# Performance work log

Hardware: AMD Instinct MI355X
Metric: run time of the kernel (lower is better)

## Reference

```python
import jax, jax.numpy as jnp
import numpy as np
from jax import lax

EPS = 1e-12


def _conv_block(x, w, scale, bias, pool):
    # x: (N, Cin, H, W), w: (Cout, Cin, 3, 3). BN in eval mode folded into scale/bias.
    y = lax.conv_general_dilated(x, w, window_strides=(1, 1), padding='SAME',
                                 dimension_numbers=('NCHW', 'OIHW', 'NCHW'))
    y = y * scale[None, :, None, None] + bias[None, :, None, None]
    y = jax.nn.relu(y)
    if pool:
        y = lax.reduce_window(y, -jnp.inf, lax.max, (1, 1, 2, 2), (1, 1, 2, 2), 'VALID')
    return y


def _encoder(x, w1, s1, b1, w2, s2, b2, w3, s3, b3, w4, s4, b4):
    x = _conv_block(x, w1, s1, b1, True)
    x = _conv_block(x, w2, s2, b2, True)
    x = _conv_block(x, w3, s3, b3, False)
    x = _conv_block(x, w4, s4, b4, False)
    return x  # (N, 64, 21, 21)


def _l2norm(x, axis):
    n = jnp.sqrt(jnp.sum(x * x, axis=axis, keepdims=True))
    return x / jnp.maximum(n, EPS)


def setup_inputs() -> dict:
    key = jax.random.key(0)
    ks = jax.random.split(key, 8)
    B, NQ, Way, Shot, C, H, W = 2, 75, 5, 5, 3, 84, 84
    D = 64
    inp = {
        'query': jax.random.normal(ks[0], (B, NQ, C, H, W), jnp.float32),
        'support': jax.random.normal(ks[1], (B, Way, Shot, C, H, W), jnp.float32),
        'w1': jax.random.normal(ks[2], (D, C, 3, 3), jnp.float32) * 0.1,
        'w2': jax.random.normal(ks[3], (D, D, 3, 3), jnp.float32) * 0.05,
        'w3': jax.random.normal(ks[4], (D, D, 3, 3), jnp.float32) * 0.05,
        'w4': jax.random.normal(ks[5], (D, D, 3, 3), jnp.float32) * 0.05,
    }
    for i in range(1, 5):
        inp[f's{i}'] = jnp.ones((D,), jnp.float32)
        inp[f'b{i}'] = jnp.zeros((D,), jnp.float32)
    return inp


def reference(query, support, w1, s1, b1, w2, s2, b2, w3, s3, b3, w4, s4, b4):
    B, NQ, C, H, W = query.shape
    _, Way, Shot, _, _, _ = support.shape
    q_flat = query.reshape(B * NQ, C, H, W)
    s_flat = support.reshape(B * Way * Shot, C, H, W)
    q_feat = _encoder(q_flat, w1, s1, b1, w2, s2, b2, w3, s3, b3, w4, s4, b4)
    s_feat = _encoder(s_flat, w1, s1, b1, w2, s2, b2, w3, s3, b3, w4, s4, b4)
    D, h, w = q_feat.shape[1], q_feat.shape[2], q_feat.shape[3]
    HW = h * w
    q_local = _l2norm(q_feat.reshape(B, NQ, D, HW), axis=2)            # (B,NQ,D,HW)
    s_local = s_feat.reshape(B, Way, Shot, D, HW).mean(axis=2)          # mean over shots
    s_local = _l2norm(s_local, axis=2)                                  # (B,Way,D,HW)
    # all pairwise local cosine similarities, batched in one einsum
    sim = jnp.einsum('bqdm,bcdn->bqcmn', q_local, s_local)              # (B,NQ,Way,HW,HW)
    best = sim.max(axis=-1)                                             # best match per query descriptor
    scores = best.mean(axis=-1)                                         # (B,NQ,Way)
    return scores.reshape(B * NQ, Way)
```

## Files before the change

### kernel.cpp

```cpp
#include <hip/hip_runtime.h>

#define EPS 1e-12f

#define NIMG   200
#define NQIMG  150
#define BDIM   2
#define NQ     75
#define WAY    5
#define SHOT   5
#define DCH    64
#define H1     84
#define H2     42
#define H3     21
#define HW1    7056
#define HW2    1764
#define HW3    441
#define PH     86
#define PSZ    7396
#define SST    448

#define PAD_BLKS  4334
#define W1_BLKS   8
#define W_BLKS    432

typedef __attribute__((ext_vector_type(8))) short bf16x8;
typedef __attribute__((ext_vector_type(4))) float f32x4;

__device__ __forceinline__ unsigned short f2bf(float f) {
    unsigned u = __float_as_uint(f);
    u += 0x7fffu + ((u >> 16) & 1u);
    return (unsigned short)(u >> 16);
}
__device__ __forceinline__ float bf2f(unsigned short h) {
    return __uint_as_float(((unsigned)h) << 16);
}
__device__ __forceinline__ int swz(int pix, int c) {
    return pix * 128 + ((c ^ ((pix >> 1) & 7)) << 4);
}

__global__ __launch_bounds__(256) void prep(
    const float* __restrict__ qin, const float* __restrict__ sin_,
    const float* __restrict__ w1, const float* __restrict__ s1,
    const float* __restrict__ w2, const float* __restrict__ s2,
    const float* __restrict__ w3, const float* __restrict__ s3,
    const float* __restrict__ w4, const float* __restrict__ s4,
    unsigned short* __restrict__ pad, unsigned short* __restrict__ p1,
    unsigned short* __restrict__ p2, unsigned short* __restrict__ p3,
    unsigned short* __restrict__ p4)
{
    int blk = blockIdx.x;
    if (blk < PAD_BLKS) {
        int idx4 = blk * 256 + threadIdx.x;
        if (idx4 >= NIMG * 3 * PSZ / 4) return;
        int idx = idx4 * 4;
        int img = idx / (3 * PSZ);
        int rem = idx % (3 * PSZ);
        int ci = rem / PSZ, p = rem % PSZ;
        const float* src = (img < NQIMG) ? (qin + (size_t)img * 3 * HW1)
                                         : (sin_ + (size_t)(img - NQIMG) * 3 * HW1);
        unsigned short o[4];
        #pragma unroll
        for (int e = 0; e < 4; e++) {
            int pe = p + e;
            int iy = pe / PH, ix = pe % PH;
            float v = 0.f;
            if (iy >= 1 && iy <= H1 && ix >= 1 && ix <= H1)
                v = src[(size_t)ci * HW1 + (iy - 1) * H1 + (ix - 1)];
            o[e] = f2bf(v);
        }
        uint2 pk;
        pk.x = (unsigned)o[0] | ((unsigned)o[1] << 16);
        pk.y = (unsigned)o[2] | ((unsigned)o[3] << 16);
        *reinterpret_cast<uint2*>(pad + idx) = pk;
    } else if (blk < PAD_BLKS + W1_BLKS) {
        int idx = (blk - PAD_BLKS) * 256 + threadIdx.x;
        int j = idx & 7, lane = (idx >> 3) & 63, mt = idx >> 9;
        int co = (mt << 4) + (lane & 15);
        int k = ((lane >> 4) << 3) + j;
        float v = 0.f;
        if (k < 27) {
            int ci = k / 9, s = k % 9;
            v = w1[(co * 3 + ci) * 9 + s] * s1[co];
        }
        p1[idx] = f2bf(v);
    } else {
        int idx = (blk - PAD_BLKS - W1_BLKS) * 256 + threadIdx.x;
        int which = idx / 36864;
        int r = idx % 36864;
        int j = r & 7, lane = (r >> 3) & 63, mt = (r >> 9) & 3, t = (r >> 11) & 1, s = r >> 12;
        int co = (mt << 4) + (lane & 15);
        int ci = (t << 5) + ((lane >> 4) << 3) + j;
        const float* w = (which == 0) ? w2 : (which == 1) ? w3 : w4;
        const float* sc = (which == 0) ? s2 : (which == 1) ? s3 : s4;
        unsigned short* p = (which == 0) ? p2 : (which == 1) ? p3 : p4;
        p[r] = f2bf(w[(co * 64 + ci) * 9 + s] * sc[co]);
    }
}

__global__ __launch_bounds__(256) void conv12_fused(
    const unsigned short* __restrict__ pad,
    const unsigned short* __restrict__ wp1, const float* __restrict__ bias1,
    const unsigned short* __restrict__ wp2, const float* __restrict__ bias2,
    unsigned short* __restrict__ out)
{
    int img = blockIdx.x / 7, tg = blockIdx.x % 7;
    int tid = threadIdx.x;
    __shared__ __attribute__((aligned(16))) unsigned short strip[3 * 18 * 86];
    __shared__ unsigned short lds2[352 * DCH];

    const unsigned* srcd = (const unsigned*)pad;
    size_t ibase = (size_t)img * 3 * (PSZ / 2);
    #pragma unroll
    for (int it = 0; it < 10; it++) {
        int i = it * 256 + tid;
        if (i < 2322) {
            int ci = i / 774, rem = i % 774;
            int sr = rem / 43, d = rem % 43;
            int y = 12 * tg - 3 + sr;
            unsigned v = 0;
            if (y >= -1 && y <= 84)
                v = srcd[ibase + ci * 3698 + (y + 1) * 43 + d];
            ((unsigned*)strip)[ci * 774 + sr * 43 + d] = v;
        }
    }
    __syncthreads();

    int wv = tid >> 6, lane = tid & 63;
    int lc = lane & 15, kg = lane >> 4;

    {
        const bf16x8* w1v = (const bf16x8*)wp1;
        bf16x8 a0 = w1v[lane];
        bf16x8 a1 = w1v[64 + lane];
        bf16x8 a2 = w1v[128 + lane];
        bf16x8 a3 = w1v[192 + lane];

        int off[8];
        #pragma unroll
        for (int j = 0; j < 8; j++) {
            int k = (kg << 3) + j;
            int kk = k < 27 ? k : 0;
            int ci = kk / 9, s = kk % 9;
            off[j] = ci * 1548 + (s / 3) * 86 + (s % 3);
        }

        f32x4 bini[4];
        #pragma unroll
        for (int mt = 0; mt < 4; mt++) {
            float4 bq = *reinterpret_cast<const float4*>(bias1 + (mt << 4) + (kg << 2));
            bini[mt] = (f32x4){bq.x, bq.y, bq.z, bq.w};
        }

        #pragma unroll
        for (int rnd = 0; rnd < 6; rnd++) {
            int pl = rnd * 64 + wv * 16 + lc;
            bool instrip = pl < 352;
            int plc = instrip ? pl : 0;
            int rr = plc / 44, cc = plc % 44;
            int pr = 6 * tg - 1 + rr, pc = cc - 1;
            bool validpx = instrip && ((unsigned)pr < (unsigned)H2) && ((unsigned)pc < (unsigned)H2);
            int ccc = ((unsigned)pc < (unsigned)H2) ? cc : 1;
            int base = (2 * rr) * 86 + (2 * ccc - 2);

            bf16x8 b[4];
            #pragma unroll
            for (int j = 0; j < 8; j++) {
                int a = base + off[j];
                b[0][j] = (short)strip[a];
                b[1][j] = (short)strip[a + 1];
                b[2][j] = (short)strip[a + 86];
                b[3][j] = (short)strip[a + 87];
            }

            f32x4 acc[4][4];
            #pragma unroll
            for (int mt = 0; mt < 4; mt++)
                #pragma unroll
                for (int sub = 0; sub < 4; sub++)
                    acc[mt][sub] = bini[mt];
            #pragma unroll
            for (int sub = 0; sub < 4; sub++) {
                acc[0][sub] = __builtin_amdgcn_mfma_f32_16x16x32_bf16(a0, b[sub], acc[0][sub], 0, 0, 0);
                acc[1][sub] = __builtin_amdgcn_mfma_f32_16x16x32_bf16(a1, b[sub], acc[1][sub], 0, 0, 0);
                acc[2][sub] = __builtin_amdgcn_mfma_f32_16x16x32_bf16(a2, b[sub], acc[2][sub], 0, 0, 0);
                acc[3][sub] = __builtin_amdgcn_mfma_f32_16x16x32_bf16(a3, b[sub], acc[3][sub], 0, 0, 0);
            }

            if (instrip) {
                #pragma unroll
                for (int mt = 0; mt < 4; mt++) {
                    uint2 pk = make_uint2(0u, 0u);
                    if (validpx) {
                        unsigned short uo[4];
                        #pragma unroll
                        for (int r = 0; r < 4; r++) {
                            float m = fmaxf(fmaxf(acc[mt][0][r], acc[mt][1][r]),
                                            fmaxf(acc[mt][2][r], acc[mt][3][r]));
                            uo[r] = f2bf(fmaxf(m, 0.f));
                        }
                        pk.x = (unsigned)uo[0] | ((unsigned)uo[1] << 16);
                        pk.y = (unsigned)uo[2] | ((unsigned)uo[3] << 16);
                    }
                    int c = (mt << 1) + (kg >> 1);
                    *(uint2*)((char*)lds2 + swz(pl, c) + ((kg & 1) << 3)) = pk;
                }
            }
        }
    }
    __syncthreads();

    int p_local = wv * 16 + lc;
    bool valid = p_local < 63;
    int pl = valid ? p_local : 62;
    int pyl = pl / 21, pxl = pl % 21;
    int pixc[4];
    #pragma unroll
    for (int sub = 0; sub < 4; sub++)
        pixc[sub] = (2 * pyl + (sub >> 1) + 1) * 44 + (2 * pxl + (sub & 1) + 1);

    f32x4 bini[4];
    #pragma unroll
    for (int mt = 0; mt < 4; mt++) {
        float4 bq = *reinterpret_cast<const float4*>(bias2 + (mt << 4) + (kg << 2));
        bini[mt] = (f32x4){bq.x, bq.y, bq.z, bq.w};
    }

    const bf16x8* wvv = (const bf16x8*)wp2;
    f32x4 acc[4][4];
    #pragma unroll
    for (int i = 0; i < 4; i++)
        #pragma unroll
        for (int j = 0; j < 4; j++)
            acc[i][j] = bini[i];

    for (int s = 0; s < 9; s++) {
        int offs = (s / 3 - 1) * 44 + (s % 3 - 1);
        #pragma unroll
        for (int t = 0; t < 2; t++) {
            int fbase = ((s * 2 + t) * 4) << 6;
            bf16x8 a0 = wvv[fbase + lane];
            bf16x8 a1 = wvv[fbase + 64 + lane];
            bf16x8 a2 = wvv[fbase + 128 + lane];
            bf16x8 a3 = wvv[fbase + 192 + lane];
            int c = (t << 2) + kg;
            bf16x8 b[4];
            #pragma unroll
            for (int sub = 0; sub < 4; sub++) {
                int pix = pixc[sub] + offs;
                b[sub] = *(const bf16x8*)((const char*)lds2 + swz(pix, c));
            }
            #pragma unroll
            for (int sub = 0; sub < 4; sub++) {
                acc[0][sub] = __builtin_amdgcn_mfma_f32_16x16x32_bf16(a0, b[sub], acc[0][sub], 0, 0, 0);
                acc[1][sub] = __builtin_amdgcn_mfma_f32_16x16x32_bf16(a1, b[sub], acc[1][sub], 0, 0, 0);
                acc[2][sub] = __builtin_amdgcn_mfma_f32_16x16x32_bf16(a2, b[sub], acc[2][sub], 0, 0, 0);
                acc[3][sub] = __builtin_amdgcn_mfma_f32_16x16x32_bf16(a3, b[sub], acc[3][sub], 0, 0, 0);
            }
        }
    }

    if (!valid) return;
    int p = tg * 63 + p_local;
    #pragma unroll
    for (int mt = 0; mt < 4; mt++) {
        unsigned short uo[4];
        #pragma unroll
        for (int r = 0; r < 4; r++) {
            float m = fmaxf(fmaxf(acc[mt][0][r], acc[mt][1][r]),
                            fmaxf(acc[mt][2][r], acc[mt][3][r]));
            uo[r] = f2bf(fmaxf(m, 0.f));
        }
        uint2 pk;
        pk.x = (unsigned)uo[0] | ((unsigned)uo[1] << 16);
        pk.y = (unsigned)uo[2] | ((unsigned)uo[3] << 16);
        *reinterpret_cast<uint2*>(out + ((size_t)img * HW3 + p) * DCH + (mt << 4) + (kg << 2)) = pk;
    }
}

__global__ __launch_bounds__(256) void conv34_fused(
    const unsigned short* __restrict__ act,
    const unsigned short* __restrict__ wp3, const unsigned short* __restrict__ wp4,
    const float* __restrict__ b3, const float* __restrict__ b4,
    unsigned short* __restrict__ a4out,
    unsigned short* __restrict__ qlout)
{
    int img = blockIdx.x;
    int tid = threadIdx.x;
    __shared__ unsigned short lds[529 * DCH];

    const unsigned short* ab = act + (size_t)img * HW3 * DCH;
    #pragma unroll
    for (int it = 0; it < 17; it++) {
        int idx = it * 256 + tid;
        if (idx < 529 * 8) {
            int pix = idx >> 3, c = idx & 7;
            int r = pix / 23, xx = pix % 23;
            int y = r - 1, x = xx - 1;
            bf16x8 v = (bf16x8)(short)0;
            if ((unsigned)y < (unsigned)H3 && (unsigned)x < (unsigned)H3)
                v = *(const bf16x8*)(ab + ((size_t)(y * H3 + x)) * DCH + (c << 3));
            *(bf16x8*)((char*)lds + swz(pix, c)) = v;
        }
    }
    __syncthreads();

    int wv = tid >> 6, lane = tid & 63;
    int lc = lane & 15, kg = lane >> 4;
    int pixBase[7];
    bool pv[7];
    #pragma unroll
    for (int i = 0; i < 7; i++) {
        int p = (wv * 7 + i) * 16 + lc;
        pv[i] = p < HW3;
        int pc = pv[i] ? p : HW3 - 1;
        pixBase[i] = (pc / 21) * 23 + (pc % 21);
    }

    f32x4 bini[4];
    #pragma unroll
    for (int mt = 0; mt < 4; mt++) {
        float4 bq = *reinterpret_cast<const float4*>(b3 + (mt << 4) + (kg << 2));
        bini[mt] = (f32x4){bq.x, bq.y, bq.z, bq.w};
    }

    f32x4 acc[7][4];
    #pragma unroll
    for (int i = 0; i < 7; i++)
        #pragma unroll
        for (int m = 0; m < 4; m++)
            acc[i][m] = bini[m];

    const bf16x8* wv3 = (const bf16x8*)wp3;
    for (int s = 0; s < 9; s++) {
        int offs = (s / 3) * 23 + (s % 3);
        #pragma unroll
        for (int t = 0; t < 2; t++) {
            int fbase = ((s * 2 + t) * 4) << 6;
            bf16x8 a0 = wv3[fbase + lane];
            bf16x8 a1 = wv3[fbase + 64 + lane];
            bf16x8 a2 = wv3[fbase + 128 + lane];
            bf16x8 a3 = wv3[fbase + 192 + lane];
            int c = (t << 2) + kg;
            #pragma unroll
            for (int i = 0; i < 7; i++) {
                int pix = pixBase[i] + offs;
                bf16x8 bb = *(const bf16x8*)((const char*)lds + swz(pix, c));
                acc[i][0] = __builtin_amdgcn_mfma_f32_16x16x32_bf16(a0, bb, acc[i][0], 0, 0, 0);
                acc[i][1] = __builtin_amdgcn_mfma_f32_16x16x32_bf16(a1, bb, acc[i][1], 0, 0, 0);
                acc[i][2] = __builtin_amdgcn_mfma_f32_16x16x32_bf16(a2, bb, acc[i][2], 0, 0, 0);
                acc[i][3] = __builtin_amdgcn_mfma_f32_16x16x32_bf16(a3, bb, acc[i][3], 0, 0, 0);
            }
        }
    }

    __syncthreads();

    #pragma unroll
    for (int i = 0; i < 7; i++) {
        if (!pv[i]) continue;
        int pix = pixBase[i] + 24;
        #pragma unroll
        for (int mt = 0; mt < 4; mt++) {
            unsigned short uo[4];
            #pragma unroll
            for (int r = 0; r < 4; r++)
                uo[r] = f2bf(fmaxf(acc[i][mt][r], 0.f));
            uint2 pk;
            pk.x = (unsigned)uo[0] | ((unsigned)uo[1] << 16);
            pk.y = (unsigned)uo[2] | ((unsigned)uo[3] << 16);
            int c = (mt << 1) + (kg >> 1);
            *(uint2*)((char*)lds + swz(pix, c) + ((kg & 1) << 3)) = pk;
        }
    }
    #pragma unroll
    for (int it = 0; it < 3; it++) {
        int idx = it * 256 + tid;
        if (idx < 704) {
            int j = idx >> 3, c = idx & 7;
            int pix;
            if (j < 23)      pix = j;
            else if (j < 46) pix = 506 + (j - 23);
            else { int k = j - 46; pix = (1 + (k >> 1)) * 23 + (k & 1) * 22; }
            *(bf16x8*)((char*)lds + swz(pix, c)) = (bf16x8)(short)0;
        }
    }
    __syncthreads();

    #pragma unroll
    for (int mt = 0; mt < 4; mt++) {
        float4 bq = *reinterpret_cast<const float4*>(b4 + (mt << 4) + (kg << 2));
        bini[mt] = (f32x4){bq.x, bq.y, bq.z, bq.w};
    }
    #pragma unroll
    for (int i = 0; i < 7; i++)
        #pragma unroll
        for (int m = 0; m < 4; m++)
            acc[i][m] = bini[m];

    const bf16x8* wv4 = (const bf16x8*)wp4;
    for (int s = 0; s < 9; s++) {
        int offs = (s / 3) * 23 + (s % 3);
        #pragma unroll
        for (int t = 0; t < 2; t++) {
            int fbase = ((s * 2 + t) * 4) << 6;
            bf16x8 a0 = wv4[fbase + lane];
            bf16x8 a1 = wv4[fbase + 64 + lane];
            bf16x8 a2 = wv4[fbase + 128 + lane];
            bf16x8 a3 = wv4[fbase + 192 + lane];
            int c = (t << 2) + kg;
            #pragma unroll
            for (int i = 0; i < 7; i++) {
                int pix = pixBase[i] + offs;
                bf16x8 bb = *(const bf16x8*)((const char*)lds + swz(pix, c));
                acc[i][0] = __builtin_amdgcn_mfma_f32_16x16x32_bf16(a0, bb, acc[i][0], 0, 0, 0);
                acc[i][1] = __builtin_amdgcn_mfma_f32_16x16x32_bf16(a1, bb, acc[i][1], 0, 0, 0);
                acc[i][2] = __builtin_amdgcn_mfma_f32_16x16x32_bf16(a2, bb, acc[i][2], 0, 0, 0);
                acc[i][3] = __builtin_amdgcn_mfma_f32_16x16x32_bf16(a3, bb, acc[i][3], 0, 0, 0);
            }
        }
    }

    if (img < NQIMG) {
        #pragma unroll
        for (int i = 0; i < 7; i++) {
            float v[4][4];
            float ssq = 0.f;
            #pragma unroll
            for (int mt = 0; mt < 4; mt++)
                #pragma unroll
                for (int r = 0; r < 4; r++) {
                    float x = fmaxf(acc[i][mt][r], 0.f);
                    v[mt][r] = x;
                    ssq = fmaf(x, x, ssq);
                }
            ssq += __shfl_xor(ssq, 16, 64);
            ssq += __shfl_xor(ssq, 32, 64);
            float inv = 1.f / fmaxf(sqrtf(ssq), EPS);
            if (!pv[i]) continue;
            int p = (wv * 7 + i) * 16 + lc;
            #pragma unroll
            for (int mt = 0; mt < 4; mt++) {
                unsigned short uo[4];
                #pragma unroll
                for (int r = 0; r < 4; r++)
                    uo[r] = f2bf(v[mt][r] * inv);
                uint2 pk;
                pk.x = (unsigned)uo[0] | ((unsigned)uo[1] << 16);
                pk.y = (unsigned)uo[2] | ((unsigned)uo[3] << 16);
                *reinterpret_cast<uint2*>(qlout + ((size_t)img * HW3 + p) * DCH + (mt << 4) + (kg << 2)) = pk;
            }
        }
    } else {
        #pragma unroll
        for (int mt = 0; mt < 4; mt++) {
            #pragma unroll
            for (int i = 0; i < 7; i++) {
                if (!pv[i]) continue;
                int p = (wv * 7 + i) * 16 + lc;
                unsigned short uo[4];
                #pragma unroll
                for (int r = 0; r < 4; r++)
                    uo[r] = f2bf(fmaxf(acc[i][mt][r], 0.f));
                uint2 pk;
                pk.x = (unsigned)uo[0] | ((unsigned)uo[1] << 16);
                pk.y = (unsigned)uo[2] | ((unsigned)uo[3] << 16);
                *reinterpret_cast<uint2*>(a4out + ((size_t)img * HW3 + p) * DCH + (mt << 4) + (kg << 2)) = pk;
            }
        }
    }
}

__global__ __launch_bounds__(256) void s_mean_norm(
    const unsigned short* __restrict__ feat, unsigned short* __restrict__ s_local)
{
    int idx = blockIdx.x * 256 + threadIdx.x;
    if (idx >= BDIM * WAY * SST) return;
    int hw = idx % SST;
    int bc = idx / SST;
    bf16x8* o = (bf16x8*)(s_local + (size_t)idx * DCH);
    if (hw >= HW3) {
        #pragma unroll
        for (int g = 0; g < 8; g++) o[g] = (bf16x8)(short)0;
        return;
    }
    int img0 = NQIMG + bc * SHOT;
    float v[DCH];
    #pragma unroll
    for (int d = 0; d < DCH; d++) v[d] = 0.f;
    for (int sh = 0; sh < SHOT; sh++) {
        const bf16x8* f = (const bf16x8*)(feat + ((size_t)(img0 + sh) * HW3 + hw) * DCH);
        #pragma unroll
        for (int g = 0; g < 8; g++) {
            bf16x8 x = f[g];
            #pragma unroll
            for (int j = 0; j < 8; j++)
                v[g * 8 + j] += bf2f((unsigned short)x[j]);
        }
    }
    float ss = 0.f;
    #pragma unroll
    for (int d = 0; d < DCH; d++) {
        v[d] *= (1.f / SHOT);
        ss = fmaf(v[d], v[d], ss);
    }
    float inv = 1.f / fmaxf(sqrtf(ss), EPS);
    #pragma unroll
    for (int g = 0; g < 8; g++) {
        bf16x8 pk;
        #pragma unroll
        for (int j = 0; j < 8; j++) pk[j] = (short)f2bf(v[g * 8 + j] * inv);
        o[g] = pk;
    }
}

__global__ __launch_bounds__(256) void sim_mfma(
    const unsigned short* __restrict__ qloc,
    const unsigned short* __restrict__ sloc,
    float* __restrict__ out)
{
    int blk = blockIdx.x;
    int imgq = blk / WAY, way = blk % WAY;
    int b = imgq / NQ;
    const unsigned short* qp = qloc + (size_t)imgq * HW3 * DCH;
    const unsigned short* sp = sloc + (size_t)(b * WAY + way) * SST * DCH;

    __shared__ unsigned short slds[SST * DCH];
    int tid = threadIdx.x;
    #pragma unroll
    for (int it = 0; it < 14; it++) {
        int idx = it * 256 + tid;
        int pix = idx >> 3, c = idx & 7;
        bf16x8 v = *(const bf16x8*)(sp + ((size_t)pix << 6) + (c << 3));
        *(bf16x8*)((char*)slds + swz(pix, c)) = v;
    }
    __syncthreads();

    int wv = tid >> 6, lane = tid & 63;
    int lc = lane & 15, kg = lane >> 4;
    int mt0 = wv * 7;

    bf16x8 qa0[7], qa1[7];
    #pragma unroll
    for (int i = 0; i < 7; i++) {
        const unsigned short* qrow = qp + (size_t)((mt0 + i) * 16 + lc) * DCH + (kg << 3);
        qa0[i] = *(const bf16x8*)(qrow);
        qa1[i] = *(const bf16x8*)(qrow + 32);
    }
    f32x4 rmax[7];
    #pragma unroll
    for (int i = 0; i < 7; i++)
        rmax[i] = (f32x4){-1e30f, -1e30f, -1e30f, -1e30f};

    const f32x4 z4 = (f32x4){0.f, 0.f, 0.f, 0.f};

    #pragma unroll
    for (int g = 0; g < 6; g++) {
        bf16x8 s0[4], s1[4];
        #pragma unroll
        for (int u = 0; u < 4; u++) {
            int pix = (4 * g + u) * 16 + lc;
            s0[u] = *(const bf16x8*)((const char*)slds + swz(pix, kg));
            s1[u] = *(const bf16x8*)((const char*)slds + swz(pix, 4 + kg));
        }
        #pragma unroll
        for (int i = 0; i < 7; i++) {
            f32x4 a[4];
            #pragma unroll
            for (int u = 0; u < 4; u++) {
                a[u] = __builtin_amdgcn_mfma_f32_16x16x32_bf16(qa0[i], s0[u], z4, 0, 0, 0);
                a[u] = __builtin_amdgcn_mfma_f32_16x16x32_bf16(qa1[i], s1[u], a[u], 0, 0, 0);
            }
            #pragma unroll
            for (int r = 0; r < 4; r++) {
                float t = fmaxf(fmaxf(rmax[i][r], a[0][r]), a[1][r]);
                rmax[i][r] = fmaxf(fmaxf(t, a[2][r]), a[3][r]);
            }
        }
    }
    {
        bf16x8 s0[4], s1[4];
        #pragma unroll
        for (int u = 0; u < 4; u++) {
            int pix = (24 + u) * 16 + lc;
            s0[u] = *(const bf16x8*)((const char*)slds + swz(pix, kg));
            s1[u] = *(const bf16x8*)((const char*)slds + swz(pix, 4 + kg));
        }
        bool nval = (432 + lc) < HW3;
        #pragma unroll
        for (int i = 0; i < 7; i++) {
            f32x4 a[4];
            #pragma unroll
            for (int u = 0; u < 4; u++) {
                a[u] = __builtin_amdgcn_mfma_f32_16x16x32_bf16(qa0[i], s0[u], z4, 0, 0, 0);
                a[u] = __builtin_amdgcn_mfma_f32_16x16x32_bf16(qa1[i], s1[u], a[u], 0, 0, 0);
            }
            #pragma unroll
            for (int r = 0; r < 4; r++) {
                float t = fmaxf(fmaxf(rmax[i][r], a[0][r]), a[1][r]);
                rmax[i][r] = fmaxf(fmaxf(t, a[2][r]), nval ? a[3][r] : -1e30f);
            }
        }
    }

    float msum = 0.f;
    #pragma unroll
    for (int i = 0; i < 7; i++) {
        #pragma unroll
        for (int r = 0; r < 4; r++) {
            float v = rmax[i][r];
            v = fmaxf(v, __shfl_xor(v, 1, 64));
            v = fmaxf(v, __shfl_xor(v, 2, 64));
            v = fmaxf(v, __shfl_xor(v, 4, 64));
            v = fmaxf(v, __shfl_xor(v, 8, 64));
            int m = (mt0 + i) * 16 + (kg << 2) + r;
            if (lc == 0 && m < HW3) msum += v;
        }
    }
    #pragma unroll
    for (int off = 32; off > 0; off >>= 1)
        msum += __shfl_xor(msum, off, 64);
    __shared__ float red[4];
    if (lane == 0) red[wv] = msum;
    __syncthreads();
    if (tid == 0)
        out[(size_t)imgq * WAY + way] = (red[0] + red[1] + red[2] + red[3]) * (1.f / HW3);
}

extern "C" void kernel_launch(void* const* d_in, const int* in_sizes, int n_in,
                              void* d_out, int out_size, void* d_ws, size_t ws_size,
                              hipStream_t stream) {
    const float* query   = (const float*)d_in[0];
    const float* support = (const float*)d_in[1];
    const float* w1 = (const float*)d_in[2];
    const float* w2 = (const float*)d_in[3];
    const float* w3 = (const float*)d_in[4];
    const float* w4 = (const float*)d_in[5];
    const float* s1 = (const float*)d_in[6];
    const float* b1 = (const float*)d_in[7];
    const float* s2 = (const float*)d_in[8];
    const float* b2 = (const float*)d_in[9];
    const float* s3 = (const float*)d_in[10];
    const float* b3 = (const float*)d_in[11];
    const float* s4 = (const float*)d_in[12];
    const float* b4 = (const float*)d_in[13];
    float* out = (float*)d_out;

    char* ws = (char*)d_ws;
    unsigned short* A2  = (unsigned short*)(ws);
    unsigned short* A4  = (unsigned short*)(ws + 11289600);
    unsigned short* QL  = (unsigned short*)(ws + 22579200);
    unsigned short* SL  = (unsigned short*)(ws + 31046400);
    unsigned short* WP2 = (unsigned short*)(ws + 31619840);
    unsigned short* WP3 = (unsigned short*)(ws + 31693568);
    unsigned short* WP4 = (unsigned short*)(ws + 31767296);
    unsigned short* WP1 = (unsigned short*)(ws + 31841024);
    unsigned short* PAD = (unsigned short*)(ws + 31845120);

    prep<<<PAD_BLKS + W1_BLKS + W_BLKS, 256, 0, stream>>>(
        query, support, w1, s1, w2, s2, w3, s3, w4, s4, PAD, WP1, WP2, WP3, WP4);

    conv12_fused<<<NIMG * 7, 256, 0, stream>>>(PAD, WP1, b1, WP2, b2, A2);
    conv34_fused<<<NIMG, 256, 0, stream>>>(A2, WP3, WP4, b3, b4, A4, QL);

    s_mean_norm<<<(BDIM * WAY * SST + 255) / 256, 256, 0, stream>>>(A4, SL);

    sim_mfma<<<NQIMG * WAY, 256, 0, stream>>>(QL, SL, out);
}
```

Measured before the change: 127.8 us.

## Use dword LDS gathers for conv1 im2col and reuse a 4x4 input window in conv2

For conv1, a second copy of the input strip is built in LDS, shifted by one bf16 element. Every tap can then be fetched as an aligned 32-bit load that yields two adjacent pixels, replacing the per-element 16-bit LDS reads. For conv2, the loop order changes to channel-half outer and tap inner. A 4x4 window of input vectors is loaded once per channel half and reused across all 9 taps and 4 pool positions, cutting 72 LDS loads per thread down to 32. This costs more LDS (the shifted strip copy), an extra barrier, and more registers held live for the window.

```diff
diff --git a/kernel.cpp b/kernel.cpp
--- a/kernel.cpp
+++ b/kernel.cpp
@@ -18,6 +18,7 @@
 #define PH     86
 #define PSZ    7396
 #define SST    448
+#define SLEN   4648
 
 #define PAD_BLKS  4334
 #define W1_BLKS   8
@@ -25,6 +26,7 @@
 
 typedef __attribute__((ext_vector_type(8))) short bf16x8;
 typedef __attribute__((ext_vector_type(4))) float f32x4;
+typedef __attribute__((ext_vector_type(4))) unsigned u32x4;
 
 __device__ __forceinline__ unsigned short f2bf(float f) {
     unsigned u = __float_as_uint(f);
@@ -105,8 +107,11 @@
 {
     int img = blockIdx.x / 7, tg = blockIdx.x % 7;
     int tid = threadIdx.x;
-    __shared__ __attribute__((aligned(16))) unsigned short strip[3 * 18 * 86];
+    __shared__ __attribute__((aligned(16))) unsigned short strips[2 * SLEN];
     __shared__ unsigned short lds2[352 * DCH];
+
+    unsigned* s_dw  = (unsigned*)strips;
+    unsigned* sB_dw = (unsigned*)(strips + SLEN);
 
     const unsigned* srcd = (const unsigned*)pad;
     size_t ibase = (size_t)img * 3 * (PSZ / 2);
@@ -120,7 +125,17 @@
             unsigned v = 0;
             if (y >= -1 && y <= 84)
                 v = srcd[ibase + ci * 3698 + (y + 1) * 43 + d];
-            ((unsigned*)strip)[ci * 774 + sr * 43 + d] = v;
+            s_dw[i] = v;
+        }
+    }
+    __syncthreads();
+    #pragma unroll
+    for (int it = 0; it < 10; it++) {
+        int k = it * 256 + tid;
+        if (k < 2322) {
+            unsigned lo = s_dw[k];
+            unsigned hi = (k + 1 < 2322) ? s_dw[k + 1] : 0u;
+            sB_dw[k] = (lo >> 16) | (hi << 16);
         }
     }
     __syncthreads();
@@ -135,13 +150,14 @@
         bf16x8 a2 = w1v[128 + lane];
         bf16x8 a3 = w1v[192 + lane];
 
-        int off[8];
+        int boff[8];
         #pragma unroll
         for (int j = 0; j < 8; j++) {
             int k = (kg << 3) + j;
             int kk = k < 27 ? k : 0;
             int ci = kk / 9, s = kk % 9;
-            off[j] = ci * 1548 + (s / 3) * 86 + (s % 3);
+            int off = ci * 1548 + (s / 3) * 86 + (s % 3);
+            boff[j] = (off & 1) ? 2 * (SLEN + off - 1) : 2 * off;
         }
 
         f32x4 bini[4];
@@ -160,17 +176,30 @@
             int pr = 6 * tg - 1 + rr, pc = cc - 1;
             bool validpx = instrip && ((unsigned)pr < (unsigned)H2) && ((unsigned)pc < (unsigned)H2);
             int ccc = ((unsigned)pc < (unsigned)H2) ? cc : 1;
-            int base = (2 * rr) * 86 + (2 * ccc - 2);
-
-            bf16x8 b[4];
-            #pragma unroll
-            for (int j = 0; j < 8; j++) {
-                int a = base + off[j];
-                b[0][j] = (short)strip[a];
-                b[1][j] = (short)strip[a + 1];
-                b[2][j] = (short)strip[a + 86];
-                b[3][j] = (short)strip[a + 87];
-            }
+            int bb2 = ((2 * rr) * 86 + (2 * ccc - 2)) * 2;
+
+            unsigned v0[4], v1[4], v2[4], v3[4];
+            #pragma unroll
+            for (int jp = 0; jp < 4; jp++) {
+                const char* p0 = (const char*)strips + bb2 + boff[2 * jp];
+                const char* p1 = (const char*)strips + bb2 + boff[2 * jp + 1];
+                unsigned dA1 = *(const unsigned*)(p0);
+                unsigned dA2 = *(const unsigned*)(p0 + 172);
+                unsigned dB1 = *(const unsigned*)(p1);
+                unsigned dB2 = *(const unsigned*)(p1 + 172);
+                v0[jp] = (dA1 & 0xffffu) | (dB1 << 16);
+                v1[jp] = (dA1 >> 16) | (dB1 & 0xffff0000u);
+                v2[jp] = (dA2 & 0xffffu) | (dB2 << 16);
+                v3[jp] = (dA2 >> 16) | (dB2 & 0xffff0000u);
+            }
+            u32x4 t0 = (u32x4){v0[0], v0[1], v0[2], v0[3]};
+            u32x4 t1 = (u32x4){v1[0], v1[1], v1[2], v1[3]};
+            u32x4 t2 = (u32x4){v2[0], v2[1], v2[2], v2[3]};
+            u32x4 t3 = (u32x4){v3[0], v3[1], v3[2], v3[3]};
+            bf16x8 B0 = *(bf16x8*)&t0;
+            bf16x8 B1 = *(bf16x8*)&t1;
+            bf16x8 B2 = *(bf16x8*)&t2;
+            bf16x8 B3 = *(bf16x8*)&t3;
 
             f32x4 acc[4][4];
             #pragma unroll
@@ -178,13 +207,22 @@
                 #pragma unroll
                 for (int sub = 0; sub < 4; sub++)
                     acc[mt][sub] = bini[mt];
-            #pragma unroll
-            for (int sub = 0; sub < 4; sub++) {
-                acc[0][sub] = __builtin_amdgcn_mfma_f32_16x16x32_bf16(a0, b[sub], acc[0][sub], 0, 0, 0);
-                acc[1][sub] = __builtin_amdgcn_mfma_f32_16x16x32_bf16(a1, b[sub], acc[1][sub], 0, 0, 0);
-                acc[2][sub] = __builtin_amdgcn_mfma_f32_16x16x32_bf16(a2, b[sub], acc[2][sub], 0, 0, 0);
-                acc[3][sub] = __builtin_amdgcn_mfma_f32_16x16x32_bf16(a3, b[sub], acc[3][sub], 0, 0, 0);
-            }
+            acc[0][0] = __builtin_amdgcn_mfma_f32_16x16x32_bf16(a0, B0, acc[0][0], 0, 0, 0);
+            acc[1][0] = __builtin_amdgcn_mfma_f32_16x16x32_bf16(a1, B0, acc[1][0], 0, 0, 0);
+            acc[2][0] = __builtin_amdgcn_mfma_f32_16x16x32_bf16(a2, B0, acc[2][0], 0, 0, 0);
+            acc[3][0] = __builtin_amdgcn_mfma_f32_16x16x32_bf16(a3, B0, acc[3][0], 0, 0, 0);
+            acc[0][1] = __builtin_amdgcn_mfma_f32_16x16x32_bf16(a0, B1, acc[0][1], 0, 0, 0);
+            acc[1][1] = __builtin_amdgcn_mfma_f32_16x16x32_bf16(a1, B1, acc[1][1], 0, 0, 0);
+            acc[2][1] = __builtin_amdgcn_mfma_f32_16x16x32_bf16(a2, B1, acc[2][1], 0, 0, 0);
+            acc[3][1] = __builtin_amdgcn_mfma_f32_16x16x32_bf16(a3, B1, acc[3][1], 0, 0, 0);
+            acc[0][2] = __builtin_amdgcn_mfma_f32_16x16x32_bf16(a0, B2, acc[0][2], 0, 0, 0);
+            acc[1][2] = __builtin_amdgcn_mfma_f32_16x16x32_bf16(a1, B2, acc[1][2], 0, 0, 0);
+            acc[2][2] = __builtin_amdgcn_mfma_f32_16x16x32_bf16(a2, B2, acc[2][2], 0, 0, 0);
+            acc[3][2] = __builtin_amdgcn_mfma_f32_16x16x32_bf16(a3, B2, acc[3][2], 0, 0, 0);
+            acc[0][3] = __builtin_amdgcn_mfma_f32_16x16x32_bf16(a0, B3, acc[0][3], 0, 0, 0);
+            acc[1][3] = __builtin_amdgcn_mfma_f32_16x16x32_bf16(a1, B3, acc[1][3], 0, 0, 0);
+            acc[2][3] = __builtin_amdgcn_mfma_f32_16x16x32_bf16(a2, B3, acc[2][3], 0, 0, 0);
+            acc[3][3] = __builtin_amdgcn_mfma_f32_16x16x32_bf16(a3, B3, acc[3][3], 0, 0, 0);
 
             if (instrip) {
                 #pragma unroll
@@ -213,10 +251,6 @@
     bool valid = p_local < 63;
     int pl = valid ? p_local : 62;
     int pyl = pl / 21, pxl = pl % 21;
-    int pixc[4];
-    #pragma unroll
-    for (int sub = 0; sub < 4; sub++)
-        pixc[sub] = (2 * pyl + (sub >> 1) + 1) * 44 + (2 * pxl + (sub & 1) + 1);
 
     f32x4 bini[4];
     #pragma unroll
@@ -233,28 +267,32 @@
         for (int j = 0; j < 4; j++)
             acc[i][j] = bini[i];
 
-    for (int s = 0; s < 9; s++) {
-        int offs = (s / 3 - 1) * 44 + (s % 3 - 1);
-        #pragma unroll
-        for (int t = 0; t < 2; t++) {
+    #pragma unroll 1
+    for (int t = 0; t < 2; t++) {
+        int c = (t << 2) + kg;
+        bf16x8 W[4][4];
+        #pragma unroll
+        for (int R = 0; R < 4; R++)
+            #pragma unroll
+            for (int C = 0; C < 4; C++) {
+                int pix = (2 * pyl + R) * 44 + (2 * pxl + C);
+                W[R][C] = *(const bf16x8*)((const char*)lds2 + swz(pix, c));
+            }
+        #pragma unroll
+        for (int s = 0; s < 9; s++) {
+            const int ky = s / 3, kx = s % 3;
             int fbase = ((s * 2 + t) * 4) << 6;
             bf16x8 a0 = wvv[fbase + lane];
             bf16x8 a1 = wvv[fbase + 64 + lane];
             bf16x8 a2 = wvv[fbase + 128 + lane];
             bf16x8 a3 = wvv[fbase + 192 + lane];
-            int c = (t << 2) + kg;
-            bf16x8 b[4];
             #pragma unroll
             for (int sub = 0; sub < 4; sub++) {
-                int pix = pixc[sub] + offs;
-                b[sub] = *(const bf16x8*)((const char*)lds2 + swz(pix, c));
-            }
-            #pragma unroll
-            for (int sub = 0; sub < 4; sub++) {
-                acc[0][sub] = __builtin_amdgcn_mfma_f32_16x16x32_bf16(a0, b[sub], acc[0][sub], 0, 0, 0);
-                acc[1][sub] = __builtin_amdgcn_mfma_f32_16x16x32_bf16(a1, b[sub], acc[1][sub], 0, 0, 0);
-                acc[2][sub] = __builtin_amdgcn_mfma_f32_16x16x32_bf16(a2, b[sub], acc[2][sub], 0, 0, 0);
-                acc[3][sub] = __builtin_amdgcn_mfma_f32_16x16x32_bf16(a3, b[sub], acc[3][sub], 0, 0, 0);
+                bf16x8 bb = W[ky + (sub >> 1)][kx + (sub & 1)];
+                acc[0][sub] = __builtin_amdgcn_mfma_f32_16x16x32_bf16(a0, bb, acc[0][sub], 0, 0, 0);
+                acc[1][sub] = __builtin_amdgcn_mfma_f32_16x16x32_bf16(a1, bb, acc[1][sub], 0, 0, 0);
+                acc[2][sub] = __builtin_amdgcn_mfma_f32_16x16x32_bf16(a2, bb, acc[2][sub], 0, 0, 0);
+                acc[3][sub] = __builtin_amdgcn_mfma_f32_16x16x32_bf16(a3, bb, acc[3][sub], 0, 0, 0);
             }
         }
     }
```

New measurement: 128.3 us. Within noise of the previous version (+0.3%).
